# Optimization experiments

Measured on AMD Instinct MI355X. Metric: run time of the kernel, lower is better.

The kernel has to match this reference:

```python
import jax, jax.numpy as jnp
import numpy as np

D_MODEL = 512
N_HEADS = 8
HEAD_DIM = D_MODEL // N_HEADS
SCALE = float(np.sqrt(HEAD_DIM))


def setup_inputs() -> dict:
    key = jax.random.key(0)
    k1, k2, k3, k4, k5, k6 = jax.random.split(key, 6)
    B, T, S = 4, 2048, 4096
    query = jax.random.normal(k1, (B, T, D_MODEL), dtype=jnp.float32)
    keys = jax.random.normal(k2, (B, S, D_MODEL), dtype=jnp.float32)
    key_padding_mask = jnp.zeros((B, S), dtype=bool)  # all valid
    # Linear params (torch nn.Linear: y = x @ W.T + b)
    lim = 1.0 / np.sqrt(D_MODEL)
    q_w = jax.random.uniform(k3, (D_MODEL, D_MODEL), jnp.float32, -lim, lim)
    q_b = jax.random.uniform(k4, (D_MODEL,), jnp.float32, -lim, lim)
    k_w = jax.random.uniform(k5, (D_MODEL, D_MODEL), jnp.float32, -lim, lim)
    k_b = jax.random.uniform(k6, (D_MODEL,), jnp.float32, -lim, lim)
    return {"query": query, "keys": keys, "key_padding_mask": key_padding_mask,
            "q_w": q_w, "q_b": q_b, "k_w": k_w, "k_b": k_b}


def reference(query, keys, key_padding_mask, q_w, q_b, k_w, k_b):
    B, T, _ = query.shape
    S = keys.shape[1]
    q = (query @ q_w.T + q_b).reshape(B, T, N_HEADS, HEAD_DIM)
    k = (keys @ k_w.T + k_b).reshape(B, S, N_HEADS, HEAD_DIM)
    # mean over heads of scaled per-head QK^T == single contraction over (h,d)
    # divided by n_heads*scale; avoids materializing [B,H,T,S].
    logits = jnp.einsum('bthd,bshd->bts', q, k) / (N_HEADS * SCALE)
    logits = jnp.where(key_padding_mask[:, None, :], -jnp.inf, logits)
    return logits
```

## Files before the change

### kernel.cpp

```cpp
#include <hip/hip_runtime.h>
#include <hip/hip_bf16.h>

using bf16 = __hip_bfloat16;
typedef __attribute__((ext_vector_type(8))) short short8;
typedef __attribute__((ext_vector_type(4))) float floatx4;
typedef __attribute__((ext_vector_type(16))) float floatx16;

#define NEG_INF (-__builtin_huge_valf())

__device__ __forceinline__ void gld_lds16(const void* g, void* l) {
  __builtin_amdgcn_global_load_lds(
      (const __attribute__((address_space(1))) unsigned int*)g,
      (__attribute__((address_space(3))) unsigned int*)l, 16, 0, 0);
}

template <int N> __device__ __forceinline__ void wait_vm() {
  asm volatile("s_waitcnt vmcnt(%0)" ::"n"(N) : "memory");
}
__device__ __forceinline__ void bar() {
  asm volatile("" ::: "memory");
  __builtin_amdgcn_s_barrier();
  asm volatile("" ::: "memory");
}

__device__ __forceinline__ void cvt8(const float4& a, const float4& b, bf16* t) {
  t[0] = __float2bfloat16(a.x); t[1] = __float2bfloat16(a.y);
  t[2] = __float2bfloat16(a.z); t[3] = __float2bfloat16(a.w);
  t[4] = __float2bfloat16(b.x); t[5] = __float2bfloat16(b.y);
  t[6] = __float2bfloat16(b.z); t[7] = __float2bfloat16(b.w);
}

__global__ __launch_bounds__(256) void cvt_in(const float* __restrict__ q,
                                              const float* __restrict__ k,
                                              const float* __restrict__ qw,
                                              const float* __restrict__ kw,
                                              bf16* __restrict__ qo, bf16* __restrict__ ko,
                                              bf16* __restrict__ qwo, bf16* __restrict__ kwo) {
  const size_t e = ((size_t)blockIdx.x * 256 + threadIdx.x) * 8;
  const float* src; bf16* dst;
  if (e < 4194304)       { src = q  + e;              dst = qo  + e; }
  else if (e < 12582912) { src = k  + (e - 4194304);  dst = ko  + (e - 4194304); }
  else if (e < 12845056) { src = qw + (e - 12582912); dst = qwo + (e - 12582912); }
  else                   { src = kw + (e - 12845056); dst = kwo + (e - 12845056); }
  float4 a = *(const float4*)src;
  float4 c = *(const float4*)(src + 4);
  bf16 t[8];
  cvt8(a, c, t);
  *(short8*)dst = *(short8*)t;
}

__device__ __forceinline__ void mfma_tile32(const bf16* sAh, const bf16* sBh,
                                            int wm, int wn, int lane,
                                            floatx16 acc[2][2]) {
  const int fm = lane & 31;
  const int fk = (lane >> 5) * 8;
  #pragma unroll
  for (int ks = 0; ks < 2; ++ks) {
    short8 a0 = *(const short8*)(sAh + (wm +  0 + fm) * 32 + ks * 16 + fk);
    short8 a1 = *(const short8*)(sAh + (wm + 32 + fm) * 32 + ks * 16 + fk);
    short8 b0 = *(const short8*)(sBh + (wn +  0 + fm) * 32 + ks * 16 + fk);
    short8 b1 = *(const short8*)(sBh + (wn + 32 + fm) * 32 + ks * 16 + fk);
    acc[0][0] = __builtin_amdgcn_mfma_f32_32x32x16_bf16(a0, b0, acc[0][0], 0, 0, 0);
    acc[0][1] = __builtin_amdgcn_mfma_f32_32x32x16_bf16(a0, b1, acc[0][1], 0, 0, 0);
    acc[1][0] = __builtin_amdgcn_mfma_f32_32x32x16_bf16(a1, b0, acc[1][0], 0, 0, 0);
    acc[1][1] = __builtin_amdgcn_mfma_f32_32x32x16_bf16(a1, b1, acc[1][1], 0, 0, 0);
  }
}

__global__ __launch_bounds__(256) void proj(const bf16* __restrict__ Xq,
                                            const bf16* __restrict__ Xk,
                                            const bf16* __restrict__ qw,
                                            const bf16* __restrict__ kw,
                                            const float* __restrict__ qb,
                                            const float* __restrict__ kb,
                                            bf16* __restrict__ qo,
                                            bf16* __restrict__ ko) {
  __shared__ bf16 sA[2][128 * 32];
  __shared__ bf16 sB[2][128 * 32];
  const int mt = blockIdx.x;
  const bool isQ = mt < 64;
  const bf16* A    = isQ ? Xq : Xk;
  const bf16* W    = isQ ? qw : kw;
  const float* bias = isQ ? qb : kb;
  bf16* outp       = isQ ? qo : ko;
  const int m0 = (isQ ? mt : mt - 64) * 128;
  const int n0 = blockIdx.y * 128;

  const int tid  = threadIdx.x;
  const int lane = tid & 63;
  const int w    = tid >> 6;
  const int wm   = (w >> 1) * 64;
  const int wn   = (w & 1) * 64;
  const int st_row = lane >> 2;
  const int st_col = (lane & 3) * 8;

  floatx16 acc[2][2];
  #pragma unroll
  for (int mi = 0; mi < 2; ++mi)
    #pragma unroll
    for (int ni = 0; ni < 2; ++ni)
      #pragma unroll
      for (int r = 0; r < 16; ++r)
        acc[mi][ni][r] = 0.f;

  for (int kt = 0; kt < 512; kt += 64) {
    #pragma unroll
    for (int h = 0; h < 2; ++h)
      #pragma unroll
      for (int j = 0; j < 2; ++j) {
        const int r = (w << 5) + (j << 4);
        gld_lds16(A + (size_t)(m0 + r + st_row) * 512 + kt + h * 32 + st_col,
                  &sA[h][r * 32]);
        gld_lds16(W + (size_t)(n0 + r + st_row) * 512 + kt + h * 32 + st_col,
                  &sB[h][r * 32]);
      }
    __syncthreads();
    #pragma unroll
    for (int h = 0; h < 2; ++h)
      mfma_tile32(sA[h], sB[h], wm, wn, lane, acc);
    __syncthreads();
  }

  const int col = lane & 31;
  const int rhi = (lane >> 5) * 4;
  #pragma unroll
  for (int ni = 0; ni < 2; ++ni) {
    const int gn = n0 + wn + ni * 32 + col;
    const float bv = bias[gn];
    #pragma unroll
    for (int mi = 0; mi < 2; ++mi)
      #pragma unroll
      for (int reg = 0; reg < 16; ++reg) {
        const int row = (reg & 3) + 8 * (reg >> 2) + rhi;
        outp[(size_t)(m0 + wm + mi * 32 + row) * 512 + gn] =
            __float2bfloat16(acc[mi][ni][reg] + bv);
      }
  }
}

__global__ __launch_bounds__(512, 2) void qk8(const bf16* __restrict__ Q,
                                              const bf16* __restrict__ Kp,
                                              const unsigned char* __restrict__ mask,
                                              float* __restrict__ out) {
  __shared__ alignas(16) char smem[2][4][16384];

  const int bid = blockIdx.x;
  const int sb  = ((bid & 7) << 6) | (bid >> 3);
  const int b   = sb >> 7;
  const int mt  = (sb >> 4) & 7;
  const int nt  = sb & 15;

  const bf16* Qb = Q  + ((size_t)b * 2048 + (size_t)mt * 256) * 512;
  const bf16* Kb = Kp + ((size_t)b * 4096 + (size_t)nt * 256) * 512;

  const int tid  = threadIdx.x;
  const int lane = tid & 63;
  const int w    = tid >> 6;
  const int wm   = w >> 2;
  const int wn   = w & 3;
  const int l15  = lane & 15;
  const int kg   = lane >> 4;
  const int aoff = l15 * 64 + ((kg << 4) ^ ((l15 & 8) << 2) ^ ((l15 & 2) << 3));

  auto stage_kh = [&](int t, int kh) {
    const int kt  = t * 64;
    char* dst = &smem[t & 1][0][0] + (w * 2 + kh) * 1024;
    const int r   = (w << 4) | (lane >> 2);
    const int swz = ((r & 8) << 2) ^ ((r & 2) << 3);
    const int cby = (kh << 6) | ((((lane & 3) << 4)) ^ swz);
    const int gc  = kt + (cby >> 1);
    gld_lds16(Qb + (size_t)(      r) * 512 + gc, dst);
    gld_lds16(Qb + (size_t)(128 + r) * 512 + gc, dst + 16384);
    gld_lds16(Kb + (size_t)(      r) * 512 + gc, dst + 32768);
    gld_lds16(Kb + (size_t)(128 + r) * 512 + gc, dst + 49152);
  };

  floatx4 acc[8][4];
  #pragma unroll
  for (int i = 0; i < 8; ++i)
    #pragma unroll
    for (int j = 0; j < 4; ++j)
      acc[i][j] = (floatx4){0.f, 0.f, 0.f, 0.f};

  stage_kh(0, 0); stage_kh(0, 1); stage_kh(1, 0);
  wait_vm<4>();
  bar();

  #pragma unroll
  for (int t = 0; t < 8; ++t) {
    const char* Ah = &smem[t & 1][wm][0];
    const char* Bh = &smem[t & 1][2 + (wn >> 1)][0] + (wn & 1) * 8192;
    #pragma unroll
    for (int kh = 0; kh < 2; ++kh) {
      short8 a[4], bb[4];
      if (kh == 0) { if (t < 7) stage_kh(t + 1, 1); }
      else         { if (t < 6) stage_kh(t + 2, 0); }
      #pragma unroll
      for (int fr = 0; fr < 4; ++fr)
        a[fr] = *(const short8*)(Ah + fr * 2048 + kh * 1024 + aoff);
      #pragma unroll
      for (int fn = 0; fn < 4; ++fn)
        bb[fn] = *(const short8*)(Bh + fn * 2048 + kh * 1024 + aoff);
      bar();
      asm volatile("s_waitcnt lgkmcnt(0)" ::: "memory");
      __builtin_amdgcn_sched_barrier(0);
      __builtin_amdgcn_s_setprio(1);
      #pragma unroll
      for (int fr = 0; fr < 4; ++fr)
        #pragma unroll
        for (int fn = 0; fn < 4; ++fn)
          acc[fr][fn] = __builtin_amdgcn_mfma_f32_16x16x32_bf16(
              a[fr], bb[fn], acc[fr][fn], 0, 0, 0);
      __builtin_amdgcn_s_setprio(0);
      bar();
      #pragma unroll
      for (int fr = 0; fr < 4; ++fr)
        a[fr] = *(const short8*)(Ah + (4 + fr) * 2048 + kh * 1024 + aoff);
      bar();
      asm volatile("s_waitcnt lgkmcnt(0)" ::: "memory");
      __builtin_amdgcn_sched_barrier(0);
      __builtin_amdgcn_s_setprio(1);
      #pragma unroll
      for (int fr = 0; fr < 4; ++fr)
        #pragma unroll
        for (int fn = 0; fn < 4; ++fn)
          acc[4 + fr][fn] = __builtin_amdgcn_mfma_f32_16x16x32_bf16(
              a[fr], bb[fn], acc[4 + fr][fn], 0, 0, 0);
      __builtin_amdgcn_s_setprio(0);
      if (kh == 1) {
        if (t < 6)       wait_vm<4>();
        else if (t == 6) wait_vm<0>();
      }
      bar();
    }
  }

  float* ob = out + (size_t)b * 2048 * 4096
                  + ((size_t)mt * 256 + (size_t)wm * 128) * 4096
                  + (size_t)nt * 256 + wn * 64;
  const unsigned char* mb = mask + (size_t)b * 4096 + nt * 256 + wn * 64;
  #pragma unroll
  for (int fc = 0; fc < 4; ++fc) {
    const int c = fc * 16 + l15;
    const bool msk = mb[c] != 0;
    #pragma unroll
    for (int f8 = 0; f8 < 8; ++f8)
      #pragma unroll
      for (int r = 0; r < 4; ++r)
        ob[(size_t)(f8 * 16 + kg * 4 + r) * 4096 + c] =
            msk ? NEG_INF : acc[f8][fc][r] * (1.f / 64.f);
  }
}

extern "C" void kernel_launch(void* const* d_in, const int* in_sizes, int n_in,
                              void* d_out, int out_size, void* d_ws, size_t ws_size,
                              hipStream_t stream) {
  const float* query = (const float*)d_in[0];
  const float* keys  = (const float*)d_in[1];
  const unsigned char* mask = (const unsigned char*)d_in[2];
  const float* q_w = (const float*)d_in[3];
  const float* q_b = (const float*)d_in[4];
  const float* k_w = (const float*)d_in[5];
  const float* k_b = (const float*)d_in[6];
  float* out = (float*)d_out;

  const size_t nq = 4194304;
  const size_t nk = 8388608;
  const size_t nw = 262144;

  char* ws = (char*)d_ws;
  bf16* q_bf   = (bf16*)ws;
  bf16* k_bf   = (bf16*)(ws + nq * 2);
  bf16* qw_bf  = (bf16*)(ws + (nq + nk) * 2);
  bf16* kw_bf  = (bf16*)(ws + (nq + nk + nw) * 2);
  bf16* q_proj = (bf16*)(ws + (nq + nk + 2 * nw) * 2);
  bf16* k_proj = (bf16*)(ws + (2 * nq + nk + 2 * nw) * 2);

  cvt_in<<<6400, 256, 0, stream>>>(query, keys, q_w, k_w, q_bf, k_bf, qw_bf, kw_bf);
  proj<<<dim3(192, 4), 256, 0, stream>>>(q_bf, k_bf, qw_bf, kw_bf, q_b, k_b,
                                         q_proj, k_proj);
  qk8<<<512, 512, 0, stream>>>(q_proj, k_proj, mask, out);
}
```

Before: 261.3 us.

## Fold Q and K projections into single Wq^T Wk matrix with rank-one bias terms

```diff
diff --git a/kernel.cpp b/kernel.cpp
--- a/kernel.cpp
+++ b/kernel.cpp
@@ -30,23 +30,120 @@
   t[6] = __float2bfloat16(b.z); t[7] = __float2bfloat16(b.w);
 }
 
+
+__global__ __launch_bounds__(256) void prep_small(const float* __restrict__ qw,
+                                                  const float* __restrict__ kw,
+                                                  const float* __restrict__ qb,
+                                                  const float* __restrict__ kb,
+                                                  float* __restrict__ w1,
+                                                  float* __restrict__ w2,
+                                                  float* __restrict__ cks) {
+  const int tid = threadIdx.x;
+  if (blockIdx.x == 0) {
+    float a0 = 0.f, a1 = 0.f;
+    for (int i = 0; i < 512; ++i) {
+      const float s = kb[i];
+      a0 += qw[(size_t)i * 512 + tid] * s;
+      a1 += qw[(size_t)i * 512 + tid + 256] * s;
+    }
+    w1[tid] = a0; w1[tid + 256] = a1;
+    __shared__ float red[256];
+    red[tid] = qb[tid] * kb[tid] + qb[tid + 256] * kb[tid + 256];
+    __syncthreads();
+    for (int s = 128; s > 0; s >>= 1) {
+      if (tid < s) red[tid] += red[tid + s];
+      __syncthreads();
+    }
+    if (tid == 0) *cks = red[0];
+  } else {
+    float a0 = 0.f, a1 = 0.f;
+    for (int i = 0; i < 512; ++i) {
+      const float s = qb[i];
+      a0 += kw[(size_t)i * 512 + tid] * s;
+      a1 += kw[(size_t)i * 512 + tid + 256] * s;
+    }
+    w2[tid] = a0; w2[tid + 256] = a1;
+  }
+}
+
+__global__ __launch_bounds__(256) void prep_m(const float* __restrict__ qw,
+                                              const float* __restrict__ kw,
+                                              bf16* __restrict__ mtp) {
+  __shared__ float skw[2][8][64];
+  __shared__ float sqw[2][8][64];
+  const int n0 = blockIdx.y * 64, k0 = blockIdx.x * 64;
+  const int tid = threadIdx.x;
+  const int tr = tid >> 4, tc = tid & 15;
+  const int sr = tid >> 5, sc = (tid & 31) * 2;
+  float acc[4][4];
+  #pragma unroll
+  for (int x = 0; x < 4; ++x)
+    #pragma unroll
+    for (int y = 0; y < 4; ++y) acc[x][y] = 0.f;
+
+  auto stage = [&](int buf, int i0) {
+    float2 kv = *(const float2*)&kw[(size_t)(i0 + sr) * 512 + n0 + sc];
+    float2 qv = *(const float2*)&qw[(size_t)(i0 + sr) * 512 + k0 + sc];
+    skw[buf][sr][sc] = kv.x; skw[buf][sr][sc + 1] = kv.y;
+    sqw[buf][sr][sc] = qv.x; sqw[buf][sr][sc + 1] = qv.y;
+  };
+  stage(0, 0);
+  __syncthreads();
+  for (int cb = 0; cb < 64; ++cb) {
+    if (cb < 63) stage((cb + 1) & 1, (cb + 1) * 8);
+    const int buf = cb & 1;
+    #pragma unroll
+    for (int ii = 0; ii < 8; ++ii) {
+      float av[4], bv[4];
+      #pragma unroll
+      for (int x = 0; x < 4; ++x) av[x] = skw[buf][ii][tr * 4 + x];
+      #pragma unroll
+      for (int y = 0; y < 4; ++y) bv[y] = sqw[buf][ii][tc * 4 + y];
+      #pragma unroll
+      for (int x = 0; x < 4; ++x)
+        #pragma unroll
+        for (int y = 0; y < 4; ++y) acc[x][y] += av[x] * bv[y];
+    }
+    __syncthreads();
+  }
+  #pragma unroll
+  for (int x = 0; x < 4; ++x)
+    #pragma unroll
+    for (int y = 0; y < 4; ++y)
+      mtp[(size_t)(n0 + tr * 4 + x) * 512 + k0 + tc * 4 + y] =
+          __float2bfloat16(acc[x][y]);
+}
+
 __global__ __launch_bounds__(256) void cvt_in(const float* __restrict__ q,
                                               const float* __restrict__ k,
-                                              const float* __restrict__ qw,
-                                              const float* __restrict__ kw,
+                                              const float* __restrict__ w1,
+                                              const float* __restrict__ w2,
+                                              const float* __restrict__ cks,
                                               bf16* __restrict__ qo, bf16* __restrict__ ko,
-                                              bf16* __restrict__ qwo, bf16* __restrict__ kwo) {
+                                              float* __restrict__ u, float* __restrict__ v) {
   const size_t e = ((size_t)blockIdx.x * 256 + threadIdx.x) * 8;
-  const float* src; bf16* dst;
-  if (e < 4194304)       { src = q  + e;              dst = qo  + e; }
-  else if (e < 12582912) { src = k  + (e - 4194304);  dst = ko  + (e - 4194304); }
-  else if (e < 12845056) { src = qw + (e - 12582912); dst = qwo + (e - 12582912); }
-  else                   { src = kw + (e - 12845056); dst = kwo + (e - 12845056); }
+  const bool isX = e < 4194304;
+  const float* src = isX ? q + e : k + (e - 4194304);
+  bf16*        dst = isX ? qo + e : ko + (e - 4194304);
+  const float* wv  = (isX ? w1 : w2) + (int)(e & 511);
+
   float4 a = *(const float4*)src;
   float4 c = *(const float4*)(src + 4);
   bf16 t[8];
   cvt8(a, c, t);
   *(short8*)dst = *(short8*)t;
+
+  float4 wa = *(const float4*)wv;
+  float4 wb = *(const float4*)(wv + 4);
+  float p = a.x * wa.x + a.y * wa.y + a.z * wa.z + a.w * wa.w +
+            c.x * wb.x + c.y * wb.y + c.z * wb.z + c.w * wb.w;
+  #pragma unroll
+  for (int d = 1; d < 64; d <<= 1) p += __shfl_xor(p, d, 64);
+  if ((threadIdx.x & 63) == 0) {
+    const size_t row = e >> 9;
+    if (isX) u[row] = p + *cks;
+    else     v[row - 8192] = p;
+  }
 }
 
 __device__ __forceinline__ void mfma_tile32(const bf16* sAh, const bf16* sBh,
@@ -67,23 +164,12 @@
   }
 }
 
-__global__ __launch_bounds__(256) void proj(const bf16* __restrict__ Xq,
-                                            const bf16* __restrict__ Xk,
-                                            const bf16* __restrict__ qw,
-                                            const bf16* __restrict__ kw,
-                                            const float* __restrict__ qb,
-                                            const float* __restrict__ kb,
-                                            bf16* __restrict__ qo,
-                                            bf16* __restrict__ ko) {
+__global__ __launch_bounds__(256) void zgemm(const bf16* __restrict__ X,
+                                             const bf16* __restrict__ Mt,
+                                             bf16* __restrict__ Z) {
   __shared__ bf16 sA[2][128 * 32];
   __shared__ bf16 sB[2][128 * 32];
-  const int mt = blockIdx.x;
-  const bool isQ = mt < 64;
-  const bf16* A    = isQ ? Xq : Xk;
-  const bf16* W    = isQ ? qw : kw;
-  const float* bias = isQ ? qb : kb;
-  bf16* outp       = isQ ? qo : ko;
-  const int m0 = (isQ ? mt : mt - 64) * 128;
+  const int m0 = blockIdx.x * 128;
   const int n0 = blockIdx.y * 128;
 
   const int tid  = threadIdx.x;
@@ -109,9 +195,9 @@
       #pragma unroll
       for (int j = 0; j < 2; ++j) {
         const int r = (w << 5) + (j << 4);
-        gld_lds16(A + (size_t)(m0 + r + st_row) * 512 + kt + h * 32 + st_col,
+        gld_lds16(X  + (size_t)(m0 + r + st_row) * 512 + kt + h * 32 + st_col,
                   &sA[h][r * 32]);
-        gld_lds16(W + (size_t)(n0 + r + st_row) * 512 + kt + h * 32 + st_col,
+        gld_lds16(Mt + (size_t)(n0 + r + st_row) * 512 + kt + h * 32 + st_col,
                   &sB[h][r * 32]);
       }
     __syncthreads();
@@ -126,14 +212,13 @@
   #pragma unroll
   for (int ni = 0; ni < 2; ++ni) {
     const int gn = n0 + wn + ni * 32 + col;
-    const float bv = bias[gn];
     #pragma unroll
     for (int mi = 0; mi < 2; ++mi)
       #pragma unroll
       for (int reg = 0; reg < 16; ++reg) {
         const int row = (reg & 3) + 8 * (reg >> 2) + rhi;
-        outp[(size_t)(m0 + wm + mi * 32 + row) * 512 + gn] =
-            __float2bfloat16(acc[mi][ni][reg] + bv);
+        Z[(size_t)(m0 + wm + mi * 32 + row) * 512 + gn] =
+            __float2bfloat16(acc[mi][ni][reg]);
       }
   }
 }
@@ -141,6 +226,8 @@
 __global__ __launch_bounds__(512, 2) void qk8(const bf16* __restrict__ Q,
                                               const bf16* __restrict__ Kp,
                                               const unsigned char* __restrict__ mask,
+                                              const float* __restrict__ u,
+                                              const float* __restrict__ v,
                                               float* __restrict__ out) {
   __shared__ alignas(16) char smem[2][4][16384];
 
@@ -239,16 +326,25 @@
                   + ((size_t)mt * 256 + (size_t)wm * 128) * 4096
                   + (size_t)nt * 256 + wn * 64;
   const unsigned char* mb = mask + (size_t)b * 4096 + nt * 256 + wn * 64;
+  const float* ub = u + (size_t)b * 2048 + mt * 256 + wm * 128;
+  const float* vb = v + (size_t)b * 4096 + nt * 256 + wn * 64;
+  float ur[8][4];
+  #pragma unroll
+  for (int f8 = 0; f8 < 8; ++f8)
+    #pragma unroll
+    for (int r = 0; r < 4; ++r)
+      ur[f8][r] = ub[f8 * 16 + kg * 4 + r];
   #pragma unroll
   for (int fc = 0; fc < 4; ++fc) {
     const int c = fc * 16 + l15;
     const bool msk = mb[c] != 0;
+    const float vc = vb[c];
     #pragma unroll
     for (int f8 = 0; f8 < 8; ++f8)
       #pragma unroll
       for (int r = 0; r < 4; ++r)
         ob[(size_t)(f8 * 16 + kg * 4 + r) * 4096 + c] =
-            msk ? NEG_INF : acc[f8][fc][r] * (1.f / 64.f);
+            msk ? NEG_INF : (acc[f8][fc][r] + ur[f8][r] + vc) * (1.f / 64.f);
   }
 }
 
@@ -264,20 +360,20 @@
   const float* k_b = (const float*)d_in[6];
   float* out = (float*)d_out;
 
-  const size_t nq = 4194304;
-  const size_t nk = 8388608;
-  const size_t nw = 262144;
-
   char* ws = (char*)d_ws;
-  bf16* q_bf   = (bf16*)ws;
-  bf16* k_bf   = (bf16*)(ws + nq * 2);
-  bf16* qw_bf  = (bf16*)(ws + (nq + nk) * 2);
-  bf16* kw_bf  = (bf16*)(ws + (nq + nk + nw) * 2);
-  bf16* q_proj = (bf16*)(ws + (nq + nk + 2 * nw) * 2);
-  bf16* k_proj = (bf16*)(ws + (2 * nq + nk + 2 * nw) * 2);
-
-  cvt_in<<<6400, 256, 0, stream>>>(query, keys, q_w, k_w, q_bf, k_bf, qw_bf, kw_bf);
-  proj<<<dim3(192, 4), 256, 0, stream>>>(q_bf, k_bf, qw_bf, kw_bf, q_b, k_b,
-                                         q_proj, k_proj);
-  qk8<<<512, 512, 0, stream>>>(q_proj, k_proj, mask, out);
-}
+  bf16*  x_bf  = (bf16*)(ws);
+  bf16*  y_bf  = (bf16*)(ws + 8388608);
+  bf16*  mt_bf = (bf16*)(ws + 25165824);
+  bf16*  z_bf  = (bf16*)(ws + 25690112);
+  float* u     = (float*)(ws + 34078720);
+  float* v     = (float*)(ws + 34111488);
+  float* w1    = (float*)(ws + 34177024);
+  float* w2    = (float*)(ws + 34179072);
+  float* cks   = (float*)(ws + 34181120);
+
+  prep_small<<<2, 256, 0, stream>>>(q_w, k_w, q_b, k_b, w1, w2, cks);
+  prep_m<<<dim3(8, 8), 256, 0, stream>>>(q_w, k_w, mt_bf);
+  cvt_in<<<6144, 256, 0, stream>>>(query, keys, w1, w2, cks, x_bf, y_bf, u, v);
+  zgemm<<<dim3(64, 4), 256, 0, stream>>>(x_bf, mt_bf, z_bf);
+  qk8<<<512, 512, 0, stream>>>(z_bf, y_bf, mask, u, v, out);
+}
```

Result: slower. 296.7 us (+13.6%).
